# Optimization experiments

Measured on AMD Instinct MI355X. Metric: run time of the kernel, lower is better.

The kernel has to match this reference:

```python
import jax, jax.numpy as jnp
import numpy as np

LAMBDA_DECAY = 0.01   # self.lambda_decay
ALPHA = 0.95          # self.alpha_continuity
TAU = 0.0             # self.tau
LN_EPS = 1e-5

M, D = 8192, 4096


def layer_norm(x):
    m = jnp.mean(x, axis=-1, keepdims=True)
    v = jnp.var(x, axis=-1, keepdims=True)
    return (x - m) / jnp.sqrt(v + LN_EPS)


def setup_inputs() -> dict:
    key = jax.random.key(0)
    k1, k2, k3, k4, k5 = jax.random.split(key, 5)
    return {
        "states": jax.random.normal(k1, (M, D), dtype=jnp.float32),       # memory bank cell states
        "weights": jax.random.uniform(k2, (M,), dtype=jnp.float32),        # per-cell weights
        "timestamps": jax.random.uniform(k3, (M,), dtype=jnp.float32),     # per-cell timestamps
        "current_state": jax.random.normal(k4, (D,), dtype=jnp.float32),
        "sensed_state": jax.random.normal(k5, (D,), dtype=jnp.float32),    # appended to bank; not in output math
        "t_new": jnp.ones((1,), dtype=jnp.float32),
    }


def reference(states, weights, timestamps, current_state, sensed_state, t_new):
    # Batched per-cell decay update (replaces the Python loop with .item() syncs):
    # cell.weight *= exp(-lambda * |(t_new - cell.timestamp) - tau|)
    decay = jnp.exp(-LAMBDA_DECAY * jnp.abs((t_new[0] - timestamps) - TAU))  # [M]
    w = weights * decay                                                       # [M]

    # scaled_dot single-query attention over the memory bank, modulated by cell weights
    scale = 1.0 / jnp.sqrt(jnp.asarray(states.shape[-1], dtype=states.dtype))
    scores = (states @ current_state) * scale        # [M]
    attn = jax.nn.softmax(scores)                    # [M]
    wa = attn * w
    wa = wa / (jnp.sum(wa) + 1e-9)                   # renormalize by decayed cell weights
    attention_out = wa @ states                      # [D]

    # recursive update: new = alpha * current + (1 - alpha) * attention_out
    new_state = ALPHA * current_state + (1.0 - ALPHA) * attention_out

    # layer norm of the new persistent state
    return layer_norm(new_state)
```

## Files before the change

kernel.cpp:

```cpp
#include <hip/hip_runtime.h>
#include <math.h>

#define LAMBDA_DECAY 0.01f
#define ALPHA 0.95f
#define LN_EPS 1e-5f

#define NB 512
#define RPB 16
#define WPB 8
#define G2 64
#define NP2 8

typedef float v4f __attribute__((ext_vector_type(4)));

static __device__ __forceinline__ float wave_sum_all(float v) {
#pragma unroll
    for (int o = 32; o > 0; o >>= 1) v += __shfl_xor(v, o);
    return v;
}

static __device__ float block_sum(float v, float* sh, int nwaves) {
    int lane = threadIdx.x & 63;
    int w = threadIdx.x >> 6;
    v = wave_sum_all(v);
    if (lane == 0) sh[w] = v;
    __syncthreads();
    float r = 0.0f;
    for (int i = 0; i < nwaves; ++i) r += sh[i];
    __syncthreads();
    return r;
}

__global__ __launch_bounds__(512) void fused_kernel(
    const float* __restrict__ states, const float* __restrict__ cur,
    const float* __restrict__ weights, const float* __restrict__ ts,
    const float* __restrict__ t_new,
    float* __restrict__ partial, float* __restrict__ partE, float* __restrict__ partS,
    int M, int D, float scale)
{
    __shared__ float shp[2][WPB];

    const int wid = threadIdx.x >> 6;
    const int lane = threadIdx.x & 63;
    const int r0 = blockIdx.x * RPB;
    const int f4base = wid * 128 + lane;
    const int rstride = D >> 2;

    const float tn = t_new[0];

    const v4f* c4 = (const v4f*)cur;
    const v4f curp0 = c4[f4base];
    const v4f curp1 = c4[f4base + 64];

    v4f acc0 = (v4f)(0.0f), acc1 = (v4f)(0.0f);
    float E = 0.0f, S = 0.0f;

    const v4f* sp = (const v4f*)states;

    v4f rv[2][2];
    rv[0][0] = sp[(size_t)r0 * rstride + f4base];
    rv[0][1] = sp[(size_t)r0 * rstride + f4base + 64];

#pragma unroll
    for (int r = 0; r < RPB; ++r) {
        const int row = r0 + r;
        const int cb = r & 1;
        const int nb = cb ^ 1;

        if (r + 1 < RPB) {
            rv[nb][0] = sp[(size_t)(row + 1) * rstride + f4base];
            rv[nb][1] = sp[(size_t)(row + 1) * rstride + f4base + 64];
        }

        const v4f a0 = rv[cb][0], a1 = rv[cb][1];

        float d0 = 0.0f, d1 = 0.0f;
        d0 = fmaf(a0[0], curp0[0], d0); d1 = fmaf(a1[0], curp1[0], d1);
        d0 = fmaf(a0[1], curp0[1], d0); d1 = fmaf(a1[1], curp1[1], d1);
        d0 = fmaf(a0[2], curp0[2], d0); d1 = fmaf(a1[2], curp1[2], d1);
        d0 = fmaf(a0[3], curp0[3], d0); d1 = fmaf(a1[3], curp1[3], d1);
        float pd = wave_sum_all(d0 + d1);

        if (lane == 0) shp[cb][wid] = pd;
        asm volatile("s_waitcnt lgkmcnt(0)" ::: "memory");
        __builtin_amdgcn_s_barrier();

        float s = 0.0f;
#pragma unroll
        for (int w = 0; w < WPB; ++w) s += shp[cb][w];
        s *= scale;

        const float e = expf(s);
        const float wgt = weights[row] * expf(-LAMBDA_DECAY * fabsf(tn - ts[row]));
        const float p = e * wgt;
        E += e; S += p;

        acc0 += p * a0;
        acc1 += p * a1;
    }

    v4f* pb = (v4f*)(partial + (size_t)blockIdx.x * D);
    pb[f4base] = acc0;
    pb[f4base + 64] = acc1;
    if (threadIdx.x == 0) {
        partE[blockIdx.x] = E;
        partS[blockIdx.x] = S;
    }
}

__global__ __launch_bounds__(256) void reduce_kernel(
    const float* __restrict__ partial, float* __restrict__ partial2, int D)
{
    const int col = blockIdx.x * 256 + threadIdx.x;
    const int b0 = blockIdx.y * G2;
    float a0 = 0.0f, a1 = 0.0f, a2 = 0.0f, a3 = 0.0f;
    for (int b = 0; b < G2; b += 4) {
        a0 += partial[(size_t)(b0 + b) * D + col];
        a1 += partial[(size_t)(b0 + b + 1) * D + col];
        a2 += partial[(size_t)(b0 + b + 2) * D + col];
        a3 += partial[(size_t)(b0 + b + 3) * D + col];
    }
    partial2[(size_t)blockIdx.y * D + col] = (a0 + a1) + (a2 + a3);
}

__global__ __launch_bounds__(1024) void finalize_kernel(
    const float* __restrict__ partial2, const float* __restrict__ partE,
    const float* __restrict__ partS, const float* __restrict__ cur,
    float* __restrict__ out, int D)
{
    __shared__ float sh[16];
    const int tid = threadIdx.x;

    float E = 0.0f, S = 0.0f;
    for (int i = tid; i < NB; i += 1024) { E += partE[i]; S += partS[i]; }
    E = block_sum(E, sh, 16);
    S = block_sum(S, sh, 16);
    const float inv = 1.0f / (S + 1e-9f * E);

    float v[4];
    float s = 0.0f, s2 = 0.0f;
#pragma unroll
    for (int k = 0; k < 4; ++k) {
        const int c = tid + k * 1024;
        float a = 0.0f;
#pragma unroll
        for (int y = 0; y < NP2; ++y) a += partial2[y * D + c];
        const float nv = ALPHA * cur[c] + (1.0f - ALPHA) * (a * inv);
        v[k] = nv;
        s += nv; s2 += nv * nv;
    }
    s = block_sum(s, sh, 16);
    s2 = block_sum(s2, sh, 16);
    const float mean = s / (float)D;
    const float var = s2 / (float)D - mean * mean;
    const float rstd = 1.0f / sqrtf(var + LN_EPS);
#pragma unroll
    for (int k = 0; k < 4; ++k)
        out[tid + k * 1024] = (v[k] - mean) * rstd;
}

extern "C" void kernel_launch(void* const* d_in, const int* in_sizes, int n_in,
                              void* d_out, int out_size, void* d_ws, size_t ws_size,
                              hipStream_t stream) {
    const float* states     = (const float*)d_in[0];
    const float* weights    = (const float*)d_in[1];
    const float* timestamps = (const float*)d_in[2];
    const float* current    = (const float*)d_in[3];
    const float* t_new      = (const float*)d_in[5];
    float* out = (float*)d_out;

    const int M = in_sizes[1];
    const int D = in_sizes[3];

    float* ws       = (float*)d_ws;
    float* partial  = ws;
    float* partial2 = partial + (size_t)NB * D;
    float* partE    = partial2 + (size_t)NP2 * D;
    float* partS    = partE + NB;

    const float scale = 1.0f / sqrtf((float)D);

    fused_kernel<<<NB, 512, 0, stream>>>(
        states, current, weights, timestamps, t_new,
        partial, partE, partS, M, D, scale);

    {
        dim3 grid(D / 256, NP2);
        reduce_kernel<<<grid, 256, 0, stream>>>(partial, partial2, D);
    }

    finalize_kernel<<<1, 1024, 0, stream>>>(partial2, partE, partS, current, out, D);
}
```

Measured before the change: 43.02 us.

## Use 256-thread blocks with 8 rows each and hoist per-row decay weights

The fused kernel now launches twice as many blocks (1024), each with 4 waves that process 8 rows, and each thread handles 16 columns of a row instead of 8. The per-row decay weights are computed up front, before the row loop, instead of inside it. The custom barrier is replaced by __syncthreads. The goal is more blocks in flight and cheaper cross-wave reductions per row. The cost is a partial buffer twice as large (1024×D), so the reduce kernel has more data to read and write.

```diff
diff --git a/kernel.cpp b/kernel.cpp
--- a/kernel.cpp
+++ b/kernel.cpp
@@ -5,10 +5,10 @@
 #define ALPHA 0.95f
 #define LN_EPS 1e-5f
 
-#define NB 512
-#define RPB 16
-#define WPB 8
-#define G2 64
+#define NB 1024
+#define RPB 8
+#define WPB 4
+#define G2 128
 #define NP2 8
 
 typedef float v4f __attribute__((ext_vector_type(4)));
@@ -31,7 +31,7 @@
     return r;
 }
 
-__global__ __launch_bounds__(512) void fused_kernel(
+__global__ __launch_bounds__(256) void fused_kernel(
     const float* __restrict__ states, const float* __restrict__ cur,
     const float* __restrict__ weights, const float* __restrict__ ts,
     const float* __restrict__ t_new,
@@ -43,65 +43,72 @@
     const int wid = threadIdx.x >> 6;
     const int lane = threadIdx.x & 63;
     const int r0 = blockIdx.x * RPB;
-    const int f4base = wid * 128 + lane;
+    const int f4base = wid * 256 + lane;
     const int rstride = D >> 2;
 
     const float tn = t_new[0];
 
     const v4f* c4 = (const v4f*)cur;
-    const v4f curp0 = c4[f4base];
-    const v4f curp1 = c4[f4base + 64];
-
-    v4f acc0 = (v4f)(0.0f), acc1 = (v4f)(0.0f);
+    v4f curp[4];
+#pragma unroll
+    for (int k = 0; k < 4; ++k) curp[k] = c4[f4base + k * 64];
+
+    float wdec[RPB];
+#pragma unroll
+    for (int r = 0; r < RPB; ++r)
+        wdec[r] = weights[r0 + r] * expf(-LAMBDA_DECAY * fabsf(tn - ts[r0 + r]));
+
+    v4f acc[4];
+#pragma unroll
+    for (int k = 0; k < 4; ++k) acc[k] = (v4f)(0.0f);
+
     float E = 0.0f, S = 0.0f;
 
-    const v4f* sp = (const v4f*)states;
-
-    v4f rv[2][2];
-    rv[0][0] = sp[(size_t)r0 * rstride + f4base];
-    rv[0][1] = sp[(size_t)r0 * rstride + f4base + 64];
+    const v4f* sp = (const v4f*)states + (size_t)r0 * rstride + f4base;
+
+    v4f rv[2][4];
+#pragma unroll
+    for (int k = 0; k < 4; ++k) rv[0][k] = sp[k * 64];
 
 #pragma unroll
     for (int r = 0; r < RPB; ++r) {
-        const int row = r0 + r;
         const int cb = r & 1;
-        const int nb = cb ^ 1;
+        const int nbuf = cb ^ 1;
 
         if (r + 1 < RPB) {
-            rv[nb][0] = sp[(size_t)(row + 1) * rstride + f4base];
-            rv[nb][1] = sp[(size_t)(row + 1) * rstride + f4base + 64];
+#pragma unroll
+            for (int k = 0; k < 4; ++k)
+                rv[nbuf][k] = sp[(size_t)(r + 1) * rstride + k * 64];
         }
 
-        const v4f a0 = rv[cb][0], a1 = rv[cb][1];
-
         float d0 = 0.0f, d1 = 0.0f;
-        d0 = fmaf(a0[0], curp0[0], d0); d1 = fmaf(a1[0], curp1[0], d1);
-        d0 = fmaf(a0[1], curp0[1], d0); d1 = fmaf(a1[1], curp1[1], d1);
-        d0 = fmaf(a0[2], curp0[2], d0); d1 = fmaf(a1[2], curp1[2], d1);
-        d0 = fmaf(a0[3], curp0[3], d0); d1 = fmaf(a1[3], curp1[3], d1);
-        float pd = wave_sum_all(d0 + d1);
+#pragma unroll
+        for (int k = 0; k < 4; k += 2) {
+            const v4f a0 = rv[cb][k], a1 = rv[cb][k + 1];
+            d0 = fmaf(a0[0], curp[k][0], d0);     d1 = fmaf(a1[0], curp[k + 1][0], d1);
+            d0 = fmaf(a0[1], curp[k][1], d0);     d1 = fmaf(a1[1], curp[k + 1][1], d1);
+            d0 = fmaf(a0[2], curp[k][2], d0);     d1 = fmaf(a1[2], curp[k + 1][2], d1);
+            d0 = fmaf(a0[3], curp[k][3], d0);     d1 = fmaf(a1[3], curp[k + 1][3], d1);
+        }
+        const float pd = wave_sum_all(d0 + d1);
 
         if (lane == 0) shp[cb][wid] = pd;
-        asm volatile("s_waitcnt lgkmcnt(0)" ::: "memory");
-        __builtin_amdgcn_s_barrier();
-
-        float s = 0.0f;
-#pragma unroll
-        for (int w = 0; w < WPB; ++w) s += shp[cb][w];
+        __syncthreads();
+
+        float s = (shp[cb][0] + shp[cb][1]) + (shp[cb][2] + shp[cb][3]);
         s *= scale;
 
         const float e = expf(s);
-        const float wgt = weights[row] * expf(-LAMBDA_DECAY * fabsf(tn - ts[row]));
-        const float p = e * wgt;
+        const float p = e * wdec[r];
         E += e; S += p;
 
-        acc0 += p * a0;
-        acc1 += p * a1;
+#pragma unroll
+        for (int k = 0; k < 4; ++k) acc[k] += p * rv[cb][k];
     }
 
     v4f* pb = (v4f*)(partial + (size_t)blockIdx.x * D);
-    pb[f4base] = acc0;
-    pb[f4base + 64] = acc1;
+#pragma unroll
+    for (int k = 0; k < 4; ++k) pb[f4base + k * 64] = acc[k];
     if (threadIdx.x == 0) {
         partE[blockIdx.x] = E;
         partS[blockIdx.x] = S;
@@ -180,7 +187,7 @@
 
     const float scale = 1.0f / sqrtf((float)D);
 
-    fused_kernel<<<NB, 512, 0, stream>>>(
+    fused_kernel<<<NB, 256, 0, stream>>>(
         states, current, weights, timestamps, t_new,
         partial, partE, partS, M, D, scale);
 
```

New measurement: 41.02 us. 1.05x faster.
